# Kernel tuning notes

Hardware: AMD Instinct MI355X
Metric: run time of the kernel (lower is better)

## Reference

```python
import jax, jax.numpy as jnp
import numpy as np

B, T, C, H = 8, 2048, 1024, 64  # batch, seq, n_embed, head_size


def setup_inputs() -> dict:
    key = jax.random.key(0)
    ks = jax.random.split(key, 6)
    k = jax.random.normal(ks[0], (B, T, C), dtype=jnp.float32)
    q = jax.random.normal(ks[1], (B, T, C), dtype=jnp.float32)
    v = jax.random.normal(ks[2], (B, T, C), dtype=jnp.float32)
    mask = jnp.ones((B, T), dtype=jnp.int32)  # key-padding mask (1 = keep)
    # nn.Linear(n_embed, head_size, bias=False) weights: [head_size, n_embed]
    s = 1.0 / np.sqrt(C)
    Wk = jax.random.uniform(ks[3], (H, C), jnp.float32, -s, s)
    Wq = jax.random.uniform(ks[4], (H, C), jnp.float32, -s, s)
    Wv = jax.random.uniform(ks[5], (H, C), jnp.float32, -s, s)
    return {"k": k, "q": q, "v": v, "mask": mask, "Wk": Wk, "Wq": Wq, "Wv": Wv}


def reference(k, q, v, mask, Wk, Wq, Wv):
    Tq = q.shape[1]
    kh = jnp.einsum('btc,hc->bth', k, Wk)   # [B,T,H]
    qh = jnp.einsum('btc,hc->bth', q, Wq)   # [B,T,H]
    vh = jnp.einsum('btc,hc->bth', v, Wv)   # [B,T,H]
    scale = kh.shape[-1] ** -0.5
    wei = jnp.einsum('bqh,bkh->bqk', qh, kh) * scale  # [B,T,T]
    # causal (tril) mask
    tril = jnp.tril(jnp.ones((Tq, Tq), dtype=bool))
    neg_inf = jnp.finfo(wei.dtype).min
    wei = jnp.where(tril[None, :, :], wei, neg_inf)
    # key-padding mask: mask [B,T] -> broadcast over query rows
    wei = jnp.where(mask[:, None, :] != 0, wei, neg_inf)
    wei = jax.nn.softmax(wei, axis=-1)
    # dropout p=0.0 (eval) -> identity
    out = jnp.einsum('bqk,bkh->bqh', wei, vh)  # [B,T,H]
    return out
```

## Files before the change

### kernel.cpp

```cpp
#include <hip/hip_runtime.h>
#include <hip/hip_bf16.h>
#include <math.h>

#define Bn 8
#define Tn 2048
#define Cn 1024
#define Hn 64
#define BTHb ((size_t)Bn * Tn * Hn)

typedef __attribute__((ext_vector_type(8))) short bf16x8;
typedef __attribute__((ext_vector_type(4))) float f32x4;

static __device__ __forceinline__ unsigned short bf16rne(float f) {
    union { float f; unsigned u; } x; x.f = f;
    return (unsigned short)((x.u + 0x7FFFu + ((x.u >> 16) & 1u)) >> 16);
}

__global__ __launch_bounds__(256) void proj_kernel(
    const float* __restrict__ k, const float* __restrict__ q,
    const float* __restrict__ v,
    const float* __restrict__ Wk, const float* __restrict__ Wq,
    const float* __restrict__ Wv,
    unsigned short* __restrict__ ws)
{
    const int which = blockIdx.y;
    const float* X = (which == 0) ? k : (which == 1) ? q : v;
    const float* W = (which == 0) ? Wk : (which == 1) ? Wq : Wv;
    unsigned short* O = ws + (size_t)which * BTHb;

    __shared__ unsigned short Xs[64][72];
    __shared__ unsigned short Wt[64][72];

    const int tid  = threadIdx.x;
    const int wave = __builtin_amdgcn_readfirstlane(tid >> 6);
    const int lane = tid & 63;
    const int m    = lane & 15;
    const int quad = lane >> 4;
    const int row0 = blockIdx.x * 64;

    const int srow = tid >> 4;
    const int sc4  = tid & 15;

    f32x4 acc[4];
#pragma unroll
    for (int t = 0; t < 4; ++t) acc[t] = (f32x4){0.f, 0.f, 0.f, 0.f};

    float4 xr[4], wr[4];
#pragma unroll
    for (int u = 0; u < 4; ++u) {
        const int row = srow + 16 * u;
        xr[u] = *(const float4*)(X + (size_t)(row0 + row) * Cn + sc4 * 4);
        wr[u] = *(const float4*)(W + (size_t)row * Cn + sc4 * 4);
    }

    for (int ct = 0; ct < 16; ++ct) {
        __syncthreads();
#pragma unroll
        for (int u = 0; u < 4; ++u) {
            const int row = srow + 16 * u;
            ushort4 xb, wb;
            xb.x = bf16rne(xr[u].x); xb.y = bf16rne(xr[u].y);
            xb.z = bf16rne(xr[u].z); xb.w = bf16rne(xr[u].w);
            wb.x = bf16rne(wr[u].x); wb.y = bf16rne(wr[u].y);
            wb.z = bf16rne(wr[u].z); wb.w = bf16rne(wr[u].w);
            *(ushort4*)&Xs[row][sc4 * 4] = xb;
            *(ushort4*)&Wt[row][sc4 * 4] = wb;
        }
        __syncthreads();

        if (ct < 15) {
#pragma unroll
            for (int u = 0; u < 4; ++u) {
                const int row = srow + 16 * u;
                xr[u] = *(const float4*)(X + (size_t)(row0 + row) * Cn
                                           + (ct + 1) * 64 + sc4 * 4);
                wr[u] = *(const float4*)(W + (size_t)row * Cn
                                           + (ct + 1) * 64 + sc4 * 4);
            }
        }

#pragma unroll
        for (int kc = 0; kc < 64; kc += 32) {
            const bf16x8 a = *(const bf16x8*)&Xs[wave * 16 + m][kc + quad * 8];
#pragma unroll
            for (int ht = 0; ht < 4; ++ht) {
                const bf16x8 bfr =
                    *(const bf16x8*)&Wt[ht * 16 + m][kc + quad * 8];
                acc[ht] = __builtin_amdgcn_mfma_f32_16x16x32_bf16(
                    a, bfr, acc[ht], 0, 0, 0);
            }
        }
    }

#pragma unroll
    for (int ht = 0; ht < 4; ++ht)
#pragma unroll
        for (int r = 0; r < 4; ++r)
            O[(size_t)(row0 + wave * 16 + quad * 4 + r) * Hn + ht * 16 + m] =
                bf16rne(acc[ht][r]);
}

__global__ __launch_bounds__(256) void attn_kernel(
    const unsigned short* __restrict__ ws,
    const int* __restrict__ mask,
    float* __restrict__ out)
{
    const unsigned short* kh = ws;
    const unsigned short* qh = ws + BTHb;
    const unsigned short* vh = ws + 2 * BTHb;

    const int b   = blockIdx.y;
    const int qt  = blockIdx.x;
    const int tid = threadIdx.x;
    const int wave = __builtin_amdgcn_readfirstlane(tid >> 6);
    const int lane = tid & 63;
    const int ln   = lane & 15;
    const int quad = lane >> 4;

    __shared__ unsigned short Ks[64][72];
    __shared__ unsigned short Vt[64][72];
    __shared__ unsigned short Ps[64][72];
    __shared__ int Msk[64];

    const int wrb = qt * 64 + wave * 16;

    bf16x8 qa[2];
#pragma unroll
    for (int kc = 0; kc < 2; ++kc)
        qa[kc] = *(const bf16x8*)(qh + ((size_t)b * Tn + wrb + ln) * Hn
                                     + kc * 32 + quad * 8);

    f32x4 oacc[4];
#pragma unroll
    for (int t = 0; t < 4; ++t) oacc[t] = (f32x4){0.f, 0.f, 0.f, 0.f};
    float mrow[4] = {-1e30f, -1e30f, -1e30f, -1e30f};
    float lrow[4] = {0.f, 0.f, 0.f, 0.f};

    const int krow = tid >> 2, kseg = tid & 3;
    const int vcol = tid & 63, vseg = tid >> 6;

    uint4 kreg[2], vreg[2];
    int mreg = 0;
    {
        const unsigned short* kp =
            kh + ((size_t)b * Tn + krow) * Hn + kseg * 16;
        kreg[0] = *(const uint4*)kp;
        kreg[1] = *(const uint4*)(kp + 8);
        const unsigned short* vp =
            vh + ((size_t)b * Tn + vcol) * Hn + vseg * 16;
        vreg[0] = *(const uint4*)vp;
        vreg[1] = *(const uint4*)(vp + 8);
        if (tid < 64) mreg = mask[(size_t)b * Tn + tid];
    }

    for (int j = 0; j <= qt; ++j) {
        __syncthreads();
        *(uint4*)&Ks[krow][kseg * 16]     = kreg[0];
        *(uint4*)&Ks[krow][kseg * 16 + 8] = kreg[1];
        {
            const unsigned short* vs = (const unsigned short*)vreg;
#pragma unroll
            for (int jj = 0; jj < 16; ++jj)
                Vt[vseg * 16 + jj][vcol] = vs[jj];
        }
        if (tid < 64) Msk[tid] = mreg;
        __syncthreads();

        if (j < qt) {
            const unsigned short* kp =
                kh + ((size_t)b * Tn + (j + 1) * 64 + krow) * Hn + kseg * 16;
            kreg[0] = *(const uint4*)kp;
            kreg[1] = *(const uint4*)(kp + 8);
            const unsigned short* vp =
                vh + ((size_t)b * Tn + (j + 1) * 64 + vcol) * Hn + vseg * 16;
            vreg[0] = *(const uint4*)vp;
            vreg[1] = *(const uint4*)(vp + 8);
            if (tid < 64) mreg = mask[(size_t)b * Tn + (j + 1) * 64 + tid];
        }

        f32x4 sacc[4];
#pragma unroll
        for (int t = 0; t < 4; ++t) sacc[t] = (f32x4){0.f, 0.f, 0.f, 0.f};
#pragma unroll
        for (int kc = 0; kc < 2; ++kc) {
#pragma unroll
            for (int nt = 0; nt < 4; ++nt) {
                const bf16x8 kb =
                    *(const bf16x8*)&Ks[nt * 16 + ln][kc * 32 + quad * 8];
                sacc[nt] = __builtin_amdgcn_mfma_f32_16x16x32_bf16(
                    qa[kc], kb, sacc[nt], 0, 0, 0);
            }
        }

        const bool fullv = (j < qt);
        float pv[4][4];
        float mt[4] = {-1e30f, -1e30f, -1e30f, -1e30f};
#pragma unroll
        for (int nt = 0; nt < 4; ++nt) {
            const bool mk = (Msk[nt * 16 + ln] != 0);
            const int kpos = j * 64 + nt * 16 + ln;
#pragma unroll
            for (int r = 0; r < 4; ++r) {
                float s = sacc[nt][r] * 0.125f;
                const bool valid =
                    mk && (fullv || kpos <= wrb + quad * 4 + r);
                s = valid ? s : -1e30f;
                pv[nt][r] = s;
                mt[r] = fmaxf(mt[r], s);
            }
        }
#pragma unroll
        for (int r = 0; r < 4; ++r) {
            mt[r] = fmaxf(mt[r], __shfl_xor(mt[r], 1));
            mt[r] = fmaxf(mt[r], __shfl_xor(mt[r], 2));
            mt[r] = fmaxf(mt[r], __shfl_xor(mt[r], 4));
            mt[r] = fmaxf(mt[r], __shfl_xor(mt[r], 8));
        }
        float alpha[4], rsum[4];
#pragma unroll
        for (int r = 0; r < 4; ++r) {
            const float mn = fmaxf(mrow[r], mt[r]);
            alpha[r] = __expf(mrow[r] - mn);
            mrow[r] = mn;
            rsum[r] = 0.f;
        }
#pragma unroll
        for (int nt = 0; nt < 4; ++nt)
#pragma unroll
            for (int r = 0; r < 4; ++r) {
                const float p = (pv[nt][r] <= -1e29f)
                                    ? 0.f
                                    : __expf(pv[nt][r] - mrow[r]);
                pv[nt][r] = p;
                rsum[r] += p;
            }
#pragma unroll
        for (int r = 0; r < 4; ++r) {
            rsum[r] += __shfl_xor(rsum[r], 1);
            rsum[r] += __shfl_xor(rsum[r], 2);
            rsum[r] += __shfl_xor(rsum[r], 4);
            rsum[r] += __shfl_xor(rsum[r], 8);
            lrow[r] = lrow[r] * alpha[r] + rsum[r];
        }
#pragma unroll
        for (int nt = 0; nt < 4; ++nt)
#pragma unroll
            for (int r = 0; r < 4; ++r) oacc[nt][r] *= alpha[r];

#pragma unroll
        for (int nt = 0; nt < 4; ++nt)
#pragma unroll
            for (int r = 0; r < 4; ++r)
                Ps[wave * 16 + quad * 4 + r][nt * 16 + ln] =
                    bf16rne(pv[nt][r]);
        asm volatile("s_waitcnt lgkmcnt(0)" ::: "memory");

#pragma unroll
        for (int kc = 0; kc < 2; ++kc) {
            const bf16x8 pa =
                *(const bf16x8*)&Ps[wave * 16 + ln][kc * 32 + quad * 8];
#pragma unroll
            for (int nt = 0; nt < 4; ++nt) {
                const bf16x8 vb =
                    *(const bf16x8*)&Vt[nt * 16 + ln][kc * 32 + quad * 8];
                oacc[nt] = __builtin_amdgcn_mfma_f32_16x16x32_bf16(
                    pa, vb, oacc[nt], 0, 0, 0);
            }
        }
    }

#pragma unroll
    for (int r = 0; r < 4; ++r) {
        const float inv = 1.0f / lrow[r];
        const size_t rowoff = ((size_t)b * Tn + wrb + quad * 4 + r) * Hn;
#pragma unroll
        for (int nt = 0; nt < 4; ++nt)
            out[rowoff + nt * 16 + ln] = oacc[nt][r] * inv;
    }
}

extern "C" void kernel_launch(void* const* d_in, const int* in_sizes, int n_in,
                              void* d_out, int out_size, void* d_ws, size_t ws_size,
                              hipStream_t stream)
{
    const float* k    = (const float*)d_in[0];
    const float* q    = (const float*)d_in[1];
    const float* v    = (const float*)d_in[2];
    const int*   mask = (const int*)d_in[3];
    const float* Wk   = (const float*)d_in[4];
    const float* Wq   = (const float*)d_in[5];
    const float* Wv   = (const float*)d_in[6];
    float* out = (float*)d_out;
    unsigned short* ws = (unsigned short*)d_ws;

    dim3 pb(256), pg(Bn * Tn / 64, 3);
    proj_kernel<<<pg, pb, 0, stream>>>(k, q, v, Wk, Wq, Wv, ws);

    dim3 ab(256), ag(Tn / 64, Bn);
    attn_kernel<<<ag, ab, 0, stream>>>(ws, mask, out);
}
```

Baseline: 281.7 us.

## Double-buffer shared memory and prefetch two chunks ahead in projection kernel

Result: no change. 279.4 us (-0.8%).

```diff
diff --git a/kernel.cpp b/kernel.cpp
--- a/kernel.cpp
+++ b/kernel.cpp
@@ -28,8 +28,8 @@
     const float* W = (which == 0) ? Wk : (which == 1) ? Wq : Wv;
     unsigned short* O = ws + (size_t)which * BTHb;
 
-    __shared__ unsigned short Xs[64][72];
-    __shared__ unsigned short Wt[64][72];
+    __shared__ unsigned short Xs[2][64][72];
+    __shared__ unsigned short Wt[2][64][72];
 
     const int tid  = threadIdx.x;
     const int wave = __builtin_amdgcn_readfirstlane(tid >> 6);
@@ -41,56 +41,75 @@
     const int srow = tid >> 4;
     const int sc4  = tid & 15;
 
+    const float* Xb = X + (size_t)(row0 + srow) * Cn + sc4 * 4;
+    const float* Wb = W + (size_t)srow * Cn + sc4 * 4;
+
     f32x4 acc[4];
 #pragma unroll
     for (int t = 0; t < 4; ++t) acc[t] = (f32x4){0.f, 0.f, 0.f, 0.f};
 
-    float4 xr[4], wr[4];
-#pragma unroll
-    for (int u = 0; u < 4; ++u) {
-        const int row = srow + 16 * u;
-        xr[u] = *(const float4*)(X + (size_t)(row0 + row) * Cn + sc4 * 4);
-        wr[u] = *(const float4*)(W + (size_t)row * Cn + sc4 * 4);
+    float4 xr0[4], wr0[4], xr1[4], wr1[4];
+
+#define LOADSET(xr, wr, c)                                                   \
+    do {                                                                     \
+        _Pragma("unroll")                                                    \
+        for (int u = 0; u < 4; ++u) {                                        \
+            xr[u] = *(const float4*)(Xb + (size_t)(16 * u) * Cn + (c) * 64); \
+            wr[u] = *(const float4*)(Wb + (size_t)(16 * u) * Cn + (c) * 64); \
+        }                                                                    \
+    } while (0)
+
+#define CONVSET(xr, wr, buf)                                                 \
+    do {                                                                     \
+        _Pragma("unroll")                                                    \
+        for (int u = 0; u < 4; ++u) {                                        \
+            const int row = srow + 16 * u;                                   \
+            ushort4 xb, wb;                                                  \
+            xb.x = bf16rne(xr[u].x); xb.y = bf16rne(xr[u].y);                \
+            xb.z = bf16rne(xr[u].z); xb.w = bf16rne(xr[u].w);                \
+            wb.x = bf16rne(wr[u].x); wb.y = bf16rne(wr[u].y);                \
+            wb.z = bf16rne(wr[u].z); wb.w = bf16rne(wr[u].w);                \
+            *(ushort4*)&Xs[buf][row][sc4 * 4] = xb;                          \
+            *(ushort4*)&Wt[buf][row][sc4 * 4] = wb;                          \
+        }                                                                    \
+    } while (0)
+
+#define MFMAS(buf)                                                           \
+    do {                                                                     \
+        _Pragma("unroll")                                                    \
+        for (int kc = 0; kc < 64; kc += 32) {                                \
+            const bf16x8 a =                                                 \
+                *(const bf16x8*)&Xs[buf][wave * 16 + m][kc + quad * 8];      \
+            _Pragma("unroll")                                                \
+            for (int ht = 0; ht < 4; ++ht) {                                 \
+                const bf16x8 bfr =                                           \
+                    *(const bf16x8*)&Wt[buf][ht * 16 + m][kc + quad * 8];    \
+                acc[ht] = __builtin_amdgcn_mfma_f32_16x16x32_bf16(           \
+                    a, bfr, acc[ht], 0, 0, 0);                               \
+            }                                                                \
+        }                                                                    \
+    } while (0)
+
+    LOADSET(xr0, wr0, 0);
+    LOADSET(xr1, wr1, 1);
+    CONVSET(xr0, wr0, 0);
+    __syncthreads();
+
+    for (int c2 = 0; c2 < 8; ++c2) {
+        const int ct = c2 * 2;
+        if (ct + 2 < 16) LOADSET(xr0, wr0, ct + 2);
+        CONVSET(xr1, wr1, 1);
+        MFMAS(0);
+        __syncthreads();
+        if (ct + 3 < 16) LOADSET(xr1, wr1, ct + 3);
+        if (ct + 2 < 16) CONVSET(xr0, wr0, 0);
+        MFMAS(1);
+        __syncthreads();
     }
 
-    for (int ct = 0; ct < 16; ++ct) {
-        __syncthreads();
-#pragma unroll
-        for (int u = 0; u < 4; ++u) {
-            const int row = srow + 16 * u;
-            ushort4 xb, wb;
-            xb.x = bf16rne(xr[u].x); xb.y = bf16rne(xr[u].y);
-            xb.z = bf16rne(xr[u].z); xb.w = bf16rne(xr[u].w);
-            wb.x = bf16rne(wr[u].x); wb.y = bf16rne(wr[u].y);
-            wb.z = bf16rne(wr[u].z); wb.w = bf16rne(wr[u].w);
-            *(ushort4*)&Xs[row][sc4 * 4] = xb;
-            *(ushort4*)&Wt[row][sc4 * 4] = wb;
-        }
-        __syncthreads();
-
-        if (ct < 15) {
-#pragma unroll
-            for (int u = 0; u < 4; ++u) {
-                const int row = srow + 16 * u;
-                xr[u] = *(const float4*)(X + (size_t)(row0 + row) * Cn
-                                           + (ct + 1) * 64 + sc4 * 4);
-                wr[u] = *(const float4*)(W + (size_t)row * Cn
-                                           + (ct + 1) * 64 + sc4 * 4);
-            }
-        }
-
-#pragma unroll
-        for (int kc = 0; kc < 64; kc += 32) {
-            const bf16x8 a = *(const bf16x8*)&Xs[wave * 16 + m][kc + quad * 8];
-#pragma unroll
-            for (int ht = 0; ht < 4; ++ht) {
-                const bf16x8 bfr =
-                    *(const bf16x8*)&Wt[ht * 16 + m][kc + quad * 8];
-                acc[ht] = __builtin_amdgcn_mfma_f32_16x16x32_bf16(
-                    a, bfr, acc[ht], 0, 0, 0);
-            }
-        }
-    }
+#undef LOADSET
+#undef CONVSET
+#undef MFMAS
 
 #pragma unroll
     for (int ht = 0; ht < 4; ++ht)
```

## Stream fp32 projection tiles into LDS via direct global-to-LDS loads with double buffering

Applied to the files above, without the earlier changes.

Result: no change. 279.5 us (-0.8%).

```diff
diff --git a/kernel.cpp b/kernel.cpp
--- a/kernel.cpp
+++ b/kernel.cpp
@@ -15,6 +15,26 @@
     union { float f; unsigned u; } x; x.f = f;
     return (unsigned short)((x.u + 0x7FFFu + ((x.u >> 16) & 1u)) >> 16);
 }
+
+static __device__ __forceinline__ unsigned short hwbf16(float f) {
+    union { __hip_bfloat16 h; unsigned short u; } c;
+    c.h = __float2bfloat16(f);
+    return c.u;
+}
+
+static __device__ __forceinline__ bf16x8 cvt8(const float4 a, const float4 b) {
+    bf16x8 r;
+    r[0] = (short)hwbf16(a.x); r[1] = (short)hwbf16(a.y);
+    r[2] = (short)hwbf16(a.z); r[3] = (short)hwbf16(a.w);
+    r[4] = (short)hwbf16(b.x); r[5] = (short)hwbf16(b.y);
+    r[6] = (short)hwbf16(b.z); r[7] = (short)hwbf16(b.w);
+    return r;
+}
+
+#define GLOAD16(gsrc, ldst)                                                  \
+    __builtin_amdgcn_global_load_lds(                                        \
+        (const __attribute__((address_space(1))) void*)(gsrc),               \
+        (__attribute__((address_space(3))) void*)(ldst), 16, 0, 0)
 
 __global__ __launch_bounds__(256) void proj_kernel(
     const float* __restrict__ k, const float* __restrict__ q,
@@ -28,8 +48,8 @@
     const float* W = (which == 0) ? Wk : (which == 1) ? Wq : Wv;
     unsigned short* O = ws + (size_t)which * BTHb;
 
-    __shared__ unsigned short Xs[64][72];
-    __shared__ unsigned short Wt[64][72];
+    __shared__ float Xs[2][64][64];
+    __shared__ float Wf[2][64][64];
 
     const int tid  = threadIdx.x;
     const int wave = __builtin_amdgcn_readfirstlane(tid >> 6);
@@ -38,59 +58,73 @@
     const int quad = lane >> 4;
     const int row0 = blockIdx.x * 64;
 
-    const int srow = tid >> 4;
-    const int sc4  = tid & 15;
+    const int lrow = lane >> 4, lcol = lane & 15;
+    const float* xsrc[4];
+    const float* wsrc[4];
+#pragma unroll
+    for (int i = 0; i < 4; ++i) {
+        const int swz = lcol ^ ((i * 4 + lrow) & 7);
+        xsrc[i] = X + (size_t)(row0 + wave * 16 + i * 4 + lrow) * Cn + swz * 4;
+        wsrc[i] = W + (size_t)(wave * 16 + i * 4 + lrow) * Cn + swz * 4;
+    }
+
+    const int s0 = (2 * quad) ^ (m & 7);
+    const int s1 = s0 ^ 1;
 
     f32x4 acc[4];
 #pragma unroll
     for (int t = 0; t < 4; ++t) acc[t] = (f32x4){0.f, 0.f, 0.f, 0.f};
 
-    float4 xr[4], wr[4];
-#pragma unroll
-    for (int u = 0; u < 4; ++u) {
-        const int row = srow + 16 * u;
-        xr[u] = *(const float4*)(X + (size_t)(row0 + row) * Cn + sc4 * 4);
-        wr[u] = *(const float4*)(W + (size_t)row * Cn + sc4 * 4);
-    }
-
-    for (int ct = 0; ct < 16; ++ct) {
-        __syncthreads();
-#pragma unroll
-        for (int u = 0; u < 4; ++u) {
-            const int row = srow + 16 * u;
-            ushort4 xb, wb;
-            xb.x = bf16rne(xr[u].x); xb.y = bf16rne(xr[u].y);
-            xb.z = bf16rne(xr[u].z); xb.w = bf16rne(xr[u].w);
-            wb.x = bf16rne(wr[u].x); wb.y = bf16rne(wr[u].y);
-            wb.z = bf16rne(wr[u].z); wb.w = bf16rne(wr[u].w);
-            *(ushort4*)&Xs[row][sc4 * 4] = xb;
-            *(ushort4*)&Wt[row][sc4 * 4] = wb;
-        }
-        __syncthreads();
-
-        if (ct < 15) {
-#pragma unroll
-            for (int u = 0; u < 4; ++u) {
-                const int row = srow + 16 * u;
-                xr[u] = *(const float4*)(X + (size_t)(row0 + row) * Cn
-                                           + (ct + 1) * 64 + sc4 * 4);
-                wr[u] = *(const float4*)(W + (size_t)row * Cn
-                                           + (ct + 1) * 64 + sc4 * 4);
-            }
-        }
-
-#pragma unroll
-        for (int kc = 0; kc < 64; kc += 32) {
-            const bf16x8 a = *(const bf16x8*)&Xs[wave * 16 + m][kc + quad * 8];
-#pragma unroll
-            for (int ht = 0; ht < 4; ++ht) {
-                const bf16x8 bfr =
-                    *(const bf16x8*)&Wt[ht * 16 + m][kc + quad * 8];
-                acc[ht] = __builtin_amdgcn_mfma_f32_16x16x32_bf16(
-                    a, bfr, acc[ht], 0, 0, 0);
-            }
-        }
-    }
+#define STAGE(p, ct)                                                         \
+    do {                                                                     \
+        _Pragma("unroll")                                                    \
+        for (int i = 0; i < 4; ++i) {                                        \
+            GLOAD16(xsrc[i] + (ct) * 64, &Xs[p][wave * 16 + i * 4][0]);      \
+            GLOAD16(wsrc[i] + (ct) * 64, &Wf[p][wave * 16 + i * 4][0]);      \
+        }                                                                    \
+    } while (0)
+
+#define COMPUTE(p)                                                           \
+    do {                                                                     \
+        _Pragma("unroll")                                                    \
+        for (int kc = 0; kc < 2; ++kc) {                                     \
+            const float4 xa0 =                                               \
+                *(const float4*)&Xs[p][wave * 16 + m][(kc * 8 + s0) * 4];    \
+            const float4 xa1 =                                               \
+                *(const float4*)&Xs[p][wave * 16 + m][(kc * 8 + s1) * 4];    \
+            const bf16x8 a = cvt8(xa0, xa1);                                 \
+            _Pragma("unroll")                                                \
+            for (int ht = 0; ht < 4; ++ht) {                                 \
+                const float4 wb0 =                                           \
+                    *(const float4*)&Wf[p][ht * 16 + m][(kc * 8 + s0) * 4];  \
+                const float4 wb1 =                                           \
+                    *(const float4*)&Wf[p][ht * 16 + m][(kc * 8 + s1) * 4];  \
+                acc[ht] = __builtin_amdgcn_mfma_f32_16x16x32_bf16(           \
+                    a, cvt8(wb0, wb1), acc[ht], 0, 0, 0);                    \
+            }                                                                \
+        }                                                                    \
+    } while (0)
+
+    STAGE(0, 0);
+
+#pragma unroll
+    for (int c = 0; c < 16; ++c) {
+        if (c + 1 < 16) {
+            STAGE((c + 1) & 1, c + 1);
+            asm volatile("s_waitcnt vmcnt(8)" ::: "memory");
+        } else {
+            asm volatile("s_waitcnt vmcnt(0)" ::: "memory");
+        }
+        __builtin_amdgcn_s_barrier();
+        __builtin_amdgcn_sched_barrier(0);
+        COMPUTE(c & 1);
+        asm volatile("s_waitcnt lgkmcnt(0)" ::: "memory");
+        __builtin_amdgcn_s_barrier();
+        __builtin_amdgcn_sched_barrier(0);
+    }
+
+#undef STAGE
+#undef COMPUTE
 
 #pragma unroll
     for (int ht = 0; ht < 4; ++ht)
```

## Preload whole bf16 weight matrix into LDS and stream X directly to MFMA

Applied to the files above, without the earlier changes.

Result: slower. 294.3 us (+4.5%).

```diff
diff --git a/kernel.cpp b/kernel.cpp
--- a/kernel.cpp
+++ b/kernel.cpp
@@ -16,7 +16,22 @@
     return (unsigned short)((x.u + 0x7FFFu + ((x.u >> 16) & 1u)) >> 16);
 }
 
-__global__ __launch_bounds__(256) void proj_kernel(
+static __device__ __forceinline__ unsigned short hwbf16(float f) {
+    union { __hip_bfloat16 h; unsigned short u; } c;
+    c.h = __float2bfloat16(f);
+    return c.u;
+}
+
+static __device__ __forceinline__ bf16x8 cvt8(const float4 a, const float4 b) {
+    bf16x8 r;
+    r[0] = (short)hwbf16(a.x); r[1] = (short)hwbf16(a.y);
+    r[2] = (short)hwbf16(a.z); r[3] = (short)hwbf16(a.w);
+    r[4] = (short)hwbf16(b.x); r[5] = (short)hwbf16(b.y);
+    r[6] = (short)hwbf16(b.z); r[7] = (short)hwbf16(b.w);
+    return r;
+}
+
+__global__ __launch_bounds__(512, 2) void proj_kernel(
     const float* __restrict__ k, const float* __restrict__ q,
     const float* __restrict__ v,
     const float* __restrict__ Wk, const float* __restrict__ Wq,
@@ -28,67 +43,46 @@
     const float* W = (which == 0) ? Wk : (which == 1) ? Wq : Wv;
     unsigned short* O = ws + (size_t)which * BTHb;
 
-    __shared__ unsigned short Xs[64][72];
-    __shared__ unsigned short Wt[64][72];
+    __shared__ unsigned short WL[8192 * 8];
 
     const int tid  = threadIdx.x;
     const int wave = __builtin_amdgcn_readfirstlane(tid >> 6);
     const int lane = tid & 63;
     const int m    = lane & 15;
     const int quad = lane >> 4;
-    const int row0 = blockIdx.x * 64;
-
-    const int srow = tid >> 4;
-    const int sc4  = tid & 15;
+    const int row0 = blockIdx.x * 128;
+
+#pragma unroll
+    for (int i = 0; i < 16; ++i) {
+        const int u    = tid + 512 * i;
+        const int kc32 = u >> 8;
+        const int ht   = (u >> 6) & 3;
+        const int l    = u & 63;
+        const float* wp =
+            W + (size_t)(ht * 16 + (l & 15)) * Cn + kc32 * 32 + (l >> 4) * 8;
+        const float4 a = *(const float4*)wp;
+        const float4 b = *(const float4*)(wp + 4);
+        *(bf16x8*)&WL[(size_t)u * 8] = cvt8(a, b);
+    }
+    __syncthreads();
+
+    const float* Xr = X + (size_t)(row0 + wave * 16 + m) * Cn;
 
     f32x4 acc[4];
 #pragma unroll
     for (int t = 0; t < 4; ++t) acc[t] = (f32x4){0.f, 0.f, 0.f, 0.f};
 
-    float4 xr[4], wr[4];
-#pragma unroll
-    for (int u = 0; u < 4; ++u) {
-        const int row = srow + 16 * u;
-        xr[u] = *(const float4*)(X + (size_t)(row0 + row) * Cn + sc4 * 4);
-        wr[u] = *(const float4*)(W + (size_t)row * Cn + sc4 * 4);
-    }
-
-    for (int ct = 0; ct < 16; ++ct) {
-        __syncthreads();
-#pragma unroll
-        for (int u = 0; u < 4; ++u) {
-            const int row = srow + 16 * u;
-            ushort4 xb, wb;
-            xb.x = bf16rne(xr[u].x); xb.y = bf16rne(xr[u].y);
-            xb.z = bf16rne(xr[u].z); xb.w = bf16rne(xr[u].w);
-            wb.x = bf16rne(wr[u].x); wb.y = bf16rne(wr[u].y);
-            wb.z = bf16rne(wr[u].z); wb.w = bf16rne(wr[u].w);
-            *(ushort4*)&Xs[row][sc4 * 4] = xb;
-            *(ushort4*)&Wt[row][sc4 * 4] = wb;
-        }
-        __syncthreads();
-
-        if (ct < 15) {
-#pragma unroll
-            for (int u = 0; u < 4; ++u) {
-                const int row = srow + 16 * u;
-                xr[u] = *(const float4*)(X + (size_t)(row0 + row) * Cn
-                                           + (ct + 1) * 64 + sc4 * 4);
-                wr[u] = *(const float4*)(W + (size_t)row * Cn
-                                           + (ct + 1) * 64 + sc4 * 4);
-            }
-        }
-
-#pragma unroll
-        for (int kc = 0; kc < 64; kc += 32) {
-            const bf16x8 a = *(const bf16x8*)&Xs[wave * 16 + m][kc + quad * 8];
-#pragma unroll
-            for (int ht = 0; ht < 4; ++ht) {
-                const bf16x8 bfr =
-                    *(const bf16x8*)&Wt[ht * 16 + m][kc + quad * 8];
-                acc[ht] = __builtin_amdgcn_mfma_f32_16x16x32_bf16(
-                    a, bfr, acc[ht], 0, 0, 0);
-            }
+#pragma unroll 8
+    for (int c = 0; c < 32; ++c) {
+        const float4 a0 = *(const float4*)(Xr + c * 32 + quad * 8);
+        const float4 a1 = *(const float4*)(Xr + c * 32 + quad * 8 + 4);
+        const bf16x8 a = cvt8(a0, a1);
+#pragma unroll
+        for (int ht = 0; ht < 4; ++ht) {
+            const bf16x8 bfr =
+                *(const bf16x8*)&WL[(size_t)((c * 4 + ht) * 64 + lane) * 8];
+            acc[ht] = __builtin_amdgcn_mfma_f32_16x16x32_bf16(
+                a, bfr, acc[ht], 0, 0, 0);
         }
     }
 
@@ -293,7 +287,7 @@
     float* out = (float*)d_out;
     unsigned short* ws = (unsigned short*)d_ws;
 
-    dim3 pb(256), pg(Bn * Tn / 64, 3);
+    dim3 pb(512), pg(Bn * Tn / 128, 3);
     proj_kernel<<<pg, pb, 0, stream>>>(k, q, v, Wk, Wq, Wv, ws);
 
     dim3 ab(256), ag(Tn / 64, Bn);
```
